# Kernel tuning notes

Hardware: AMD Instinct MI355X
Metric: run time of the kernel (lower is better)

Reference implementation:

```python
import jax, jax.numpy as jnp
import numpy as np
from jax import lax

IN_DIM = 128
B, H, W = 4, 64, 64


def setup_inputs() -> dict:
    key = jax.random.key(0)
    ks = jax.random.split(key, 11)
    C = IN_DIM
    c8 = C // 8
    s = lambda k, shape, scale: jax.random.normal(k, shape, dtype=jnp.float32) * scale
    return {
        "x": s(ks[0], (B, C, H, W), 1.0),
        "x_forward": s(ks[1], (B, C, H, W), 1.0),
        "x_backward": s(ks[2], (B, C, H, W), 1.0),
        # 1x1 conv weights stored as [out, in]
        "Wq": s(ks[3], (c8, C), C ** -0.5),
        "bq": jnp.zeros((c8,), jnp.float32),
        "Wk": s(ks[4], (c8, C), C ** -0.5),
        "bk": jnp.zeros((c8,), jnp.float32),
        "Wv": s(ks[5], (C, C), C ** -0.5),
        "bv": jnp.zeros((C,), jnp.float32),
        # 3x3 conv weight [out=C, in=2C, kh, kw]
        "Wf": s(ks[6], (C, 2 * C, 3, 3), (2 * C * 9) ** -0.5),
        "bf": jnp.zeros((C,), jnp.float32),
    }


def _conv1x1(x, w, b):
    # x: [B,C,H,W], w: [O,C] -> [B,O,H,W]
    return jnp.einsum("bchw,oc->bohw", x, w) + b[None, :, None, None]


def reference(x, x_forward, x_backward, Wq, bq, Wk, bk, Wv, bv, Wf, bf):
    Bb, C, Hh, Ww = x.shape
    HW = Hh * Ww
    query = _conv1x1(x_forward, Wq, bq).reshape(Bb, -1, HW)   # [B,c8,HW]
    key = _conv1x1(x, Wk, bk).reshape(Bb, -1, HW)             # [B,c8,HW]
    value = _conv1x1(x_backward, Wv, bv).reshape(Bb, C, HW)   # [B,C,HW]

    # att_score[b, k_pos, q_pos] = key[b,:,k_pos] . query[b,:,q_pos]
    att_score = jnp.einsum("bck,bcq->bkq", key, query)        # [B,HW,HW]
    max_value = jnp.max(att_score, axis=-1)                   # [B,HW]
    idx = jnp.argmax(att_score, axis=-1)                      # [B,HW] int

    selected_value = jnp.take_along_axis(value, idx[:, None, :], axis=2)
    selected_value = selected_value.reshape(Bb, C, Hh, Ww)
    max_value = max_value.reshape(Bb, 1, Hh, Ww)

    front_res = jnp.concatenate([x, selected_value], axis=1)  # [B,2C,H,W]
    front_res = lax.conv_general_dilated(
        front_res, Wf, window_strides=(1, 1), padding="SAME",
        dimension_numbers=("NCHW", "OIHW", "NCHW"),
    ) + bf[None, :, None, None]
    front_res = front_res * max_value
    return x + front_res
```

## Files before the change

### kernel.cpp

```cpp
#include <hip/hip_runtime.h>

#define HW 4096
#define CC 128
#define MARGIN 2e-3f

typedef unsigned short ushort_t;
typedef unsigned int uint_t;
typedef __attribute__((ext_vector_type(8))) short short8;
typedef __attribute__((ext_vector_type(4))) float f32x4;

__device__ __forceinline__ float dot4(float4 a, float4 b) {
    return (a.x*b.x + a.y*b.y) + (a.z*b.z + a.w*b.w);
}

__device__ __forceinline__ ushort_t f2bf(float f) {
    union { float f; uint_t u; } cv; cv.f = f;
    uint_t r = cv.u + 0x7fffu + ((cv.u >> 16) & 1u);
    return (ushort_t)(r >> 16);
}

__device__ __forceinline__ float bf2f(ushort_t h) {
    union { uint_t u; float f; } cv; cv.u = ((uint_t)h) << 16;
    return cv.f;
}

__device__ __forceinline__ void store16(ushort_t* dst, const ushort_t* s) {
    union { ushort_t s[8]; uint4 v; } a, b;
    #pragma unroll
    for (int j = 0; j < 8; j++) { a.s[j] = s[j]; b.s[j] = s[8+j]; }
    *(uint4*)dst = a.v;
    *(uint4*)(dst + 8) = b.v;
}

__device__ __forceinline__ void gl2lds16(const ushort_t* g, ushort_t* l) {
    __builtin_amdgcn_global_load_lds(
        (const __attribute__((address_space(1))) unsigned int*)g,
        (__attribute__((address_space(3))) unsigned int*)l, 16, 0, 0);
}

__global__ __launch_bounds__(256) void prep_kernel(
    const float* __restrict__ x, const float* __restrict__ xf,
    const float* __restrict__ Wq, const float* __restrict__ bq,
    const float* __restrict__ Wk, const float* __restrict__ bk,
    const float* __restrict__ Wf,
    float* __restrict__ Qt, float* __restrict__ Kt,
    ushort_t* __restrict__ Qs, ushort_t* __restrict__ KB,
    ushort_t* __restrict__ xsel, ushort_t* __restrict__ Wt)
{
    __shared__ __align__(16) unsigned char smem[16704];
    int bid = blockIdx.x;
    int tid = threadIdx.x;

    if (bid < 128) {
        bool isQ = bid < 64;
        const float* src  = isQ ? xf : x;
        const float* W    = isQ ? Wq : Wk;
        const float* bias = isQ ? bq : bk;

        int pg = (bid & 63) * 256 + tid;
        int b = pg >> 12, p = pg & 4095;
        const float* sp = src + ((size_t)b << 19) + p;

        float acc[16];
        #pragma unroll
        for (int o = 0; o < 16; o++) acc[o] = bias[o];

        for (int c4 = 0; c4 < 128; c4 += 4) {
            float x0 = sp[(size_t)(c4+0) << 12];
            float x1 = sp[(size_t)(c4+1) << 12];
            float x2 = sp[(size_t)(c4+2) << 12];
            float x3 = sp[(size_t)(c4+3) << 12];
            #pragma unroll
            for (int o = 0; o < 16; o++) {
                float4 w = *(const float4*)&W[o*128 + c4];
                acc[o] += w.x*x0 + w.y*x1 + w.z*x2 + w.w*x3;
            }
        }

        float* dstF = isQ ? Qt : Kt;
        float4* df = (float4*)(dstF + (size_t)pg * 16);
        df[0] = make_float4(acc[0],acc[1],acc[2],acc[3]);
        df[1] = make_float4(acc[4],acc[5],acc[6],acc[7]);
        df[2] = make_float4(acc[8],acc[9],acc[10],acc[11]);
        df[3] = make_float4(acc[12],acc[13],acc[14],acc[15]);

        ushort_t h[16], m[16], l[16];
        #pragma unroll
        for (int d = 0; d < 16; d++) {
            h[d] = f2bf(acc[d]);
            float r1 = acc[d] - bf2f(h[d]);
            m[d] = f2bf(r1);
            l[d] = f2bf(r1 - bf2f(m[d]));
        }
        if (isQ) {
            ushort_t* o_ = Qs + (size_t)pg*64;
            store16(o_,      h);
            store16(o_ + 16, m);
            store16(o_ + 32, h);
            store16(o_ + 48, l);
        } else {
            int u = b*256 + (p >> 4);
            int n = p & 15;
            ushort_t* o_ = KB + (size_t)u*1536 + n*32;
            store16(o_,        h); store16(o_ + 16,   h);
            store16(o_ + 512,  m); store16(o_ + 528,  m);
            store16(o_ + 1024, l); store16(o_ + 1040, h);
        }
    } else if (bid < 384) {
        ushort_t* sT = (ushort_t*)smem;
        int xbid = bid - 128;
        int b = xbid >> 6, y = xbid & 63;
        int cq = tid >> 6, xx = tid & 63;
        const float* src = x + ((size_t)b << 19) + (y << 6) + xx;
        #pragma unroll 4
        for (int k = 0; k < 32; k++) {
            int c = cq*32 + k;
            sT[xx*130 + c] = f2bf(src[(size_t)c << 12]);
        }
        __syncthreads();
        uint_t* dst = (uint_t*)(xsel + ((size_t)(b*4356 + (y+1)*66 + 1))*256);
        #pragma unroll
        for (int k = 0; k < 16; k++) {
            int idx = k*256 + tid;
            int s = idx >> 6, u = idx & 63;
            uint_t v = *(const uint_t*)&sT[s*130 + u*2];
            dst[s*128 + u] = v;
        }
    } else if (bid < 514) {
        int g = (bid - 384) * 256 + tid;
        if (g < 33280) {
            int b = g / 8320;
            int rem = g - b * 8320;
            int si = rem >> 5;
            int ch = rem & 31;
            int y, xx;
            if (si < 66)      { y = 0;  xx = si; }
            else if (si < 132){ y = 65; xx = si - 66; }
            else { int t = si - 132; y = 1 + (t >> 1); xx = (t & 1) ? 65 : 0; }
            int site = y * 66 + xx;
            uint4* dst = (uint4*)(xsel + ((size_t)(b*4356 + site))*256);
            dst[ch] = make_uint4(0,0,0,0);
        }
    } else {
        int t = (bid - 514) * 256 + tid;
        if (t < 36864) {
            int cg = t & 3;
            int o = (t >> 2) & 31;
            int tc = t >> 7;
            int tap = tc % 9;
            int rest = tc / 9;
            int cb = rest & 7, og = rest >> 3;
            union { ushort_t s[8]; uint4 v; } pk;
            #pragma unroll
            for (int j = 0; j < 8; j++) {
                int ci = cg*8 + j;
                pk.s[j] = f2bf(Wf[(size_t)(og*32 + o)*2304 + (cb*32 + ci)*9 + tap]);
            }
            *(uint4*)(Wt + (size_t)t*8) = pk.v;
        }
    }
}

__global__ __launch_bounds__(256) void v_kernel(
    const float* __restrict__ xb, const float* __restrict__ Wv,
    const float* __restrict__ bv, float* __restrict__ V)
{
    __shared__ __align__(16) float sW[32*128];
    int bid = blockIdx.x;
    int b = bid >> 6, og = (bid >> 4) & 3, pt = bid & 15;
    int tid = threadIdx.x;
    for (int e = tid; e < 4096; e += 256) sW[e] = Wv[og*4096 + e];
    __syncthreads();

    int oz = tid >> 7, pz = tid & 127;
    int p0 = pt*256 + pz, p1 = p0 + 128;
    const float* sp = xb + ((size_t)b << 19);

    float acc0[16], acc1[16];
    #pragma unroll
    for (int j = 0; j < 16; j++) { acc0[j] = 0.f; acc1[j] = 0.f; }

    for (int c4 = 0; c4 < 128; c4 += 4) {
        float a0 = sp[((size_t)(c4+0)<<12) + p0], a1 = sp[((size_t)(c4+1)<<12) + p0];
        float a2 = sp[((size_t)(c4+2)<<12) + p0], a3 = sp[((size_t)(c4+3)<<12) + p0];
        float b0 = sp[((size_t)(c4+0)<<12) + p1], b1 = sp[((size_t)(c4+1)<<12) + p1];
        float b2 = sp[((size_t)(c4+2)<<12) + p1], b3 = sp[((size_t)(c4+3)<<12) + p1];
        #pragma unroll
        for (int j = 0; j < 16; j++) {
            float4 w = *(const float4*)&sW[(oz*16 + j)*128 + c4];
            acc0[j] += w.x*a0 + w.y*a1 + w.z*a2 + w.w*a3;
            acc1[j] += w.x*b0 + w.y*b1 + w.z*b2 + w.w*b3;
        }
    }
    int obase = og*32 + oz*16;
    float* r0 = V + ((size_t)((b<<12) + p0))*128 + obase;
    float* r1 = V + ((size_t)((b<<12) + p1))*128 + obase;
    #pragma unroll
    for (int jq = 0; jq < 4; jq++) {
        float b0v = bv[obase + jq*4 + 0], b1v = bv[obase + jq*4 + 1];
        float b2v = bv[obase + jq*4 + 2], b3v = bv[obase + jq*4 + 3];
        *(float4*)(r0 + jq*4) = make_float4(acc0[jq*4]+b0v, acc0[jq*4+1]+b1v, acc0[jq*4+2]+b2v, acc0[jq*4+3]+b3v);
        *(float4*)(r1 + jq*4) = make_float4(acc1[jq*4]+b0v, acc1[jq*4+1]+b1v, acc1[jq*4+2]+b2v, acc1[jq*4+3]+b3v);
    }
}

__global__ __launch_bounds__(512, 2) void att_kernel(
    const ushort_t* __restrict__ Qs, const ushort_t* __restrict__ KB,
    float* __restrict__ maxv, int* __restrict__ idxv,
    int* __restrict__ gN, int* __restrict__ gList)
{
    __shared__ float sM1[64*33];
    __shared__ int   sI1[64*33];
    __shared__ float sM2[64*33];

    int bid = blockIdx.x;
    int kg = bid & 63, b = bid >> 6;
    int tid = threadIdx.x;
    int wave = tid >> 6, lane = tid & 63;
    int l15 = lane & 15, quad = lane >> 4;

    short8 Bf[4][3];
    const ushort_t* kb = KB + ((size_t)((b*256 + kg*4)*3))*512 + l15*32 + quad*8;
    #pragma unroll
    for (int t = 0; t < 4; t++)
        #pragma unroll
        for (int p = 0; p < 3; p++)
            Bf[t][p] = *(const short8*)(kb + (size_t)(t*3 + p)*512);

    const ushort_t* qbase = Qs + ((size_t)(b*4096 + wave*512 + l15))*64 + quad*8;

    float m1[4], m2[4]; int i1[4];
    #pragma unroll
    for (int t = 0; t < 4; t++) { m1[t] = -1e30f; m2[t] = -1e30f; i1[t] = 0; }

    for (int it = 0; it < 32; it++) {
        const ushort_t* aptr = qbase + it*1024;
        short8 A1 = *(const short8*)aptr;
        short8 A2 = *(const short8*)(aptr + 32);
        f32x4 acc[4];
        #pragma unroll
        for (int t = 0; t < 4; t++) {
            acc[t] = (f32x4)0.f;
            acc[t] = __builtin_amdgcn_mfma_f32_16x16x32_bf16(A1, Bf[t][0], acc[t], 0, 0, 0);
            acc[t] = __builtin_amdgcn_mfma_f32_16x16x32_bf16(A1, Bf[t][1], acc[t], 0, 0, 0);
            acc[t] = __builtin_amdgcn_mfma_f32_16x16x32_bf16(A2, Bf[t][2], acc[t], 0, 0, 0);
        }
        int q0 = wave*512 + it*16 + quad*4;
        #pragma unroll
        for (int r = 0; r < 4; r++) {
            int cand = q0 + r;
            #pragma unroll
            for (int t = 0; t < 4; t++) {
                float d = acc[t][r];
                float old1 = m1[t];
                bool gt = d > old1;
                m1[t] = gt ? d : old1;
                i1[t] = gt ? cand : i1[t];
                m2[t] = __builtin_amdgcn_fmed3f(d, old1, m2[t]);
            }
        }
    }

    #pragma unroll
    for (int t = 0; t < 4; t++) {
        int kl_ = t*16 + l15;
        int slot = wave*4 + quad;
        sM1[kl_*33 + slot] = m1[t];
        sI1[kl_*33 + slot] = i1[t];
        sM2[kl_*33 + slot] = m2[t];
    }
    __syncthreads();
    if (tid < 64) {
        float M1 = -1e30f; int I1 = 0x7fffffff;
        for (int s = 0; s < 32; s++) {
            float m = sM1[tid*33 + s]; int i = sI1[tid*33 + s];
            if (m > M1 || (m == M1 && i < I1)) { M1 = m; I1 = i; }
        }
        float M2 = -1e30f;
        for (int s = 0; s < 32; s++) {
            float m = sM1[tid*33 + s]; int i = sI1[tid*33 + s];
            float cnd = (i == I1) ? sM2[tid*33 + s] : m;
            M2 = fmaxf(M2, cnd);
        }
        int row = (b << 12) + kg*64 + tid;
        maxv[row] = M1; idxv[row] = I1;
        if (M1 - M2 < MARGIN) {
            int p = atomicAdd(gN, 1);
            gList[p] = row;
        }
    }
}

__global__ __launch_bounds__(256) void fixup2_kernel(
    const float* __restrict__ Qt, const float* __restrict__ Kt,
    const int* __restrict__ gN, const int* __restrict__ gList,
    float* __restrict__ maxv, int* __restrict__ idxv)
{
    __shared__ float sRm[256];
    __shared__ int   sRi[256];
    int n = *gN;
    int tid = threadIdx.x;
    for (int e = blockIdx.x; e < n; e += 64) {
        int r2 = gList[e];
        int b2 = r2 >> 12, k2 = r2 & 4095;
        const float4* Kp = (const float4*)(Kt + ((size_t)(b2*4096 + k2))*16);
        float4 ka = Kp[0], kbv = Kp[1], kc = Kp[2], kd = Kp[3];
        const float4* Qp = (const float4*)(Qt + ((size_t)b2*4096)*16);
        float m = -1e30f; int i = 0;
        #pragma unroll 4
        for (int j = 0; j < 16; j++) {
            int q = tid*16 + j;
            float4 qa = Qp[q*4+0], qb = Qp[q*4+1], qc = Qp[q*4+2], qd = Qp[q*4+3];
            float d = (dot4(ka,qa) + dot4(kbv,qb)) + (dot4(kc,qc) + dot4(kd,qd));
            if (d > m) { m = d; i = q; }
        }
        sRm[tid] = m; sRi[tid] = i;
        __syncthreads();
        #pragma unroll
        for (int s = 128; s > 0; s >>= 1) {
            if (tid < s) {
                float mo = sRm[tid+s]; int io = sRi[tid+s];
                if (mo > sRm[tid] || (mo == sRm[tid] && io < sRi[tid])) {
                    sRm[tid] = mo; sRi[tid] = io;
                }
            }
            __syncthreads();
        }
        if (tid == 0) { maxv[r2] = sRm[0]; idxv[r2] = sRi[0]; }
        __syncthreads();
    }
}

__global__ __launch_bounds__(256) void gather_kernel(
    const float* __restrict__ V, const int* __restrict__ idxv,
    ushort_t* __restrict__ xsel)
{
    int bid = blockIdx.x;
    int b = bid >> 6, pt = bid & 63;
    int tid = threadIdx.x;
    int pp = tid >> 2, cq = tid & 3;
    int p = pt*64 + pp;
    int ip = idxv[(b << 12) + p];
    const float* vrow = V + ((size_t)((b << 12) + ip))*128 + cq*32;
    int site = ((p >> 6) + 1)*66 + (p & 63) + 1;
    ushort_t* dst = xsel + ((size_t)(b*4356 + site))*256 + 128 + cq*32;
    #pragma unroll
    for (int k = 0; k < 4; k++) {
        float4 a = *(const float4*)(vrow + k*8);
        float4 c = *(const float4*)(vrow + k*8 + 4);
        union { ushort_t s[8]; uint4 v; } pk;
        pk.s[0] = f2bf(a.x); pk.s[1] = f2bf(a.y); pk.s[2] = f2bf(a.z); pk.s[3] = f2bf(a.w);
        pk.s[4] = f2bf(c.x); pk.s[5] = f2bf(c.y); pk.s[6] = f2bf(c.z); pk.s[7] = f2bf(c.w);
        *(uint4*)(dst + k*8) = pk.v;
    }
}

__global__ __launch_bounds__(256) void conv_kernel(
    const float* __restrict__ x, const ushort_t* __restrict__ xsel,
    const ushort_t* __restrict__ Wt, const float* __restrict__ bf,
    const float* __restrict__ maxv, float* __restrict__ out)
{
    __shared__ __align__(16) ushort_t sIn[336*32];
    __shared__ __align__(16) ushort_t sW[9*32*32];

    int bid = blockIdx.x;
    int og = bid & 3, tx = (bid >> 2) & 3, ty = (bid >> 4) & 3, b = bid >> 6;
    int tid = threadIdx.x;
    int wave = tid >> 6, lane = tid & 63;
    int l15 = lane & 15, quad = lane >> 4;

    const ushort_t* xsel_base = xsel + ((size_t)(b*4356 + (ty*16)*66 + tx*16))*256;
    const ushort_t* wt_base   = Wt + (size_t)og*8*9216;

    f32x4 acc[4][2];
    #pragma unroll
    for (int mi = 0; mi < 4; mi++)
        #pragma unroll
        for (int ni = 0; ni < 2; ni++) acc[mi][ni] = (f32x4)0.f;

    int l4q = lane >> 2, l4 = lane & 3;

    for (int cb = 0; cb < 8; cb++) {
        if (cb) __syncthreads();
        for (int r = wave; r < 21; r += 4) {
            int site = r*16 + l4q;
            int iy = site / 18, ix = site - iy*18;
            const ushort_t* g = xsel_base + (size_t)(iy*66 + ix)*256 + cb*32 + l4*8;
            gl2lds16(g, &sIn[r*512]);
        }
        for (int r = wave; r < 18; r += 4) {
            const ushort_t* g = wt_base + (size_t)cb*9216 + r*512 + lane*8;
            gl2lds16(g, &sW[r*512]);
        }
        __syncthreads();

        #pragma unroll
        for (int tap = 0; tap < 9; tap++) {
            const int dy = tap / 3, dx = tap % 3;
            short8 B0 = *(const short8*)&sW[(tap*32 +      l15)*32 + quad*8];
            short8 B1 = *(const short8*)&sW[(tap*32 + 16 + l15)*32 + quad*8];
            #pragma unroll
            for (int mi = 0; mi < 4; mi++) {
                int row = wave*4 + mi + dy;
                short8 A = *(const short8*)&sIn[(row*18 + l15 + dx)*32 + quad*8];
                acc[mi][0] = __builtin_amdgcn_mfma_f32_16x16x32_bf16(A, B0, acc[mi][0], 0, 0, 0);
                acc[mi][1] = __builtin_amdgcn_mfma_f32_16x16x32_bf16(A, B1, acc[mi][1], 0, 0, 0);
            }
        }
    }

    int y0 = ty*16, x0 = tx*16;
    const float* xb_ = x   + ((size_t)b << 19);
    float*       ob  = out + ((size_t)b << 19);
    const float* mxb = maxv + (b << 12);
    #pragma unroll
    for (int mi = 0; mi < 4; mi++) {
        int y = y0 + wave*4 + mi;
        int p = (y << 6) + x0 + quad*4;
        float4 mv = *(const float4*)&mxb[p];
        #pragma unroll
        for (int ni = 0; ni < 2; ni++) {
            int o = og*32 + ni*16 + l15;
            float bfo = bf[o];
            float4 xv = *(const float4*)&xb_[((size_t)o << 12) + p];
            float4 r;
            r.x = xv.x + mv.x * (acc[mi][ni][0] + bfo);
            r.y = xv.y + mv.y * (acc[mi][ni][1] + bfo);
            r.z = xv.z + mv.z * (acc[mi][ni][2] + bfo);
            r.w = xv.w + mv.w * (acc[mi][ni][3] + bfo);
            *(float4*)&ob[((size_t)o << 12) + p] = r;
        }
    }
}

extern "C" void kernel_launch(void* const* d_in, const int* in_sizes, int n_in,
                              void* d_out, int out_size, void* d_ws, size_t ws_size,
                              hipStream_t stream) {
    (void)in_sizes; (void)n_in; (void)out_size; (void)ws_size;
    const float* x  = (const float*)d_in[0];
    const float* xf = (const float*)d_in[1];
    const float* xb = (const float*)d_in[2];
    const float* Wq = (const float*)d_in[3];
    const float* bq = (const float*)d_in[4];
    const float* Wk = (const float*)d_in[5];
    const float* bk = (const float*)d_in[6];
    const float* Wv = (const float*)d_in[7];
    const float* bv = (const float*)d_in[8];
    const float* Wf = (const float*)d_in[9];
    const float* bf = (const float*)d_in[10];
    float* out = (float*)d_out;

    float* ws   = (float*)d_ws;
    float* Qt   = ws;
    float* Kt   = Qt + 262144;
    float* V    = Kt + 262144;
    float* mx   = V  + 2097152;
    int*   idxv = (int*)(mx + 16384);
    int*   gN   = (int*)(idxv + 16384);
    int*   gList= gN + 4;
    ushort_t* Qs   = (ushort_t*)(gList + 16384);
    ushort_t* KB   = Qs + 1048576;
    ushort_t* xsel = KB + 1572864;
    ushort_t* Wt   = xsel + 4460544;

    hipMemsetAsync(gN, 0, sizeof(int), stream);
    hipLaunchKernelGGL(prep_kernel,   dim3(658), dim3(256), 0, stream,
                       x, xf, Wq, bq, Wk, bk, Wf, Qt, Kt, Qs, KB, xsel, Wt);
    hipLaunchKernelGGL(v_kernel,      dim3(256), dim3(256), 0, stream, xb, Wv, bv, V);
    hipLaunchKernelGGL(att_kernel,    dim3(256), dim3(512), 0, stream, Qs, KB, mx, idxv, gN, gList);
    hipLaunchKernelGGL(fixup2_kernel, dim3(64),  dim3(256), 0, stream, Qt, Kt, gN, gList, mx, idxv);
    hipLaunchKernelGGL(gather_kernel, dim3(256), dim3(256), 0, stream, V, idxv, xsel);
    hipLaunchKernelGGL(conv_kernel,   dim3(256), dim3(256), 0, stream, x, xsel, Wt, bf, mx, out);
}
```

Baseline: 204.7 us.

## Fold V projection into prep kernel and split Q/K channel reduction across threads

Merges the separate value-projection kernel into the prep kernel as extra blocks, so one launch covers Q/K, V, padding, transpose and weight repacking. The Q/K projection now uses twice as many blocks, with each half-block reducing half the channels and combining partial sums through shared memory. V blocks are re-tiled to 8 outputs per thread over 1024 blocks. The aim is to remove a launch and its serialization and to raise parallelism in the small projection stages. In exchange it adds a block-level sync, reloads x_backward once per output group, and leaves half the Q/K threads idle during the epilogue.

```diff
diff --git a/kernel.cpp b/kernel.cpp
--- a/kernel.cpp
+++ b/kernel.cpp
@@ -39,11 +39,12 @@
 }
 
 __global__ __launch_bounds__(256) void prep_kernel(
-    const float* __restrict__ x, const float* __restrict__ xf,
+    const float* __restrict__ x, const float* __restrict__ xf, const float* __restrict__ xb,
     const float* __restrict__ Wq, const float* __restrict__ bq,
     const float* __restrict__ Wk, const float* __restrict__ bk,
+    const float* __restrict__ Wv, const float* __restrict__ bv,
     const float* __restrict__ Wf,
-    float* __restrict__ Qt, float* __restrict__ Kt,
+    float* __restrict__ Qt, float* __restrict__ Kt, float* __restrict__ V,
     ushort_t* __restrict__ Qs, ushort_t* __restrict__ KB,
     ushort_t* __restrict__ xsel, ushort_t* __restrict__ Wt)
 {
@@ -51,19 +52,87 @@
     int bid = blockIdx.x;
     int tid = threadIdx.x;
 
-    if (bid < 128) {
-        bool isQ = bid < 64;
+    if (bid < 256) {
+        bool isQ = bid < 128;
+        int sub = bid & 127;
+        int b = sub >> 5, pt = sub & 31;
         const float* src  = isQ ? xf : x;
         const float* W    = isQ ? Wq : Wk;
         const float* bias = isQ ? bq : bk;
-
-        int pg = (bid & 63) * 256 + tid;
-        int b = pg >> 12, p = pg & 4095;
-        const float* sp = src + ((size_t)b << 19) + p;
+        int ph = tid >> 7, pl = tid & 127;
+        int p = pt*128 + pl;
+        int pg = (b << 12) + p;
+        const float* sp = src + ((size_t)b << 19) + p + ((size_t)(ph*64) << 12);
 
         float acc[16];
         #pragma unroll
-        for (int o = 0; o < 16; o++) acc[o] = bias[o];
+        for (int o = 0; o < 16; o++) acc[o] = ph ? 0.f : bias[o];
+
+        for (int cc = 0; cc < 64; cc += 4) {
+            float x0 = sp[(size_t)(cc+0) << 12];
+            float x1 = sp[(size_t)(cc+1) << 12];
+            float x2 = sp[(size_t)(cc+2) << 12];
+            float x3 = sp[(size_t)(cc+3) << 12];
+            #pragma unroll
+            for (int o = 0; o < 16; o++) {
+                float4 w = *(const float4*)&W[o*128 + ph*64 + cc];
+                acc[o] += w.x*x0 + w.y*x1 + w.z*x2 + w.w*x3;
+            }
+        }
+
+        float* sAcc = (float*)smem;
+        if (ph) {
+            #pragma unroll
+            for (int o = 0; o < 16; o++) sAcc[pl*17 + o] = acc[o];
+        }
+        __syncthreads();
+        if (!ph) {
+            #pragma unroll
+            for (int o = 0; o < 16; o++) acc[o] += sAcc[pl*17 + o];
+
+            float* dstF = isQ ? Qt : Kt;
+            float4* df = (float4*)(dstF + (size_t)pg * 16);
+            df[0] = make_float4(acc[0],acc[1],acc[2],acc[3]);
+            df[1] = make_float4(acc[4],acc[5],acc[6],acc[7]);
+            df[2] = make_float4(acc[8],acc[9],acc[10],acc[11]);
+            df[3] = make_float4(acc[12],acc[13],acc[14],acc[15]);
+
+            ushort_t h[16], m[16], l[16];
+            #pragma unroll
+            for (int d = 0; d < 16; d++) {
+                h[d] = f2bf(acc[d]);
+                float r1 = acc[d] - bf2f(h[d]);
+                m[d] = f2bf(r1);
+                l[d] = f2bf(r1 - bf2f(m[d]));
+            }
+            if (isQ) {
+                ushort_t* o_ = Qs + (size_t)pg*64;
+                store16(o_,      h);
+                store16(o_ + 16, m);
+                store16(o_ + 32, h);
+                store16(o_ + 48, l);
+            } else {
+                int u = b*256 + (p >> 4);
+                int n = p & 15;
+                ushort_t* o_ = KB + (size_t)u*1536 + n*32;
+                store16(o_,        h); store16(o_ + 16,   h);
+                store16(o_ + 512,  m); store16(o_ + 528,  m);
+                store16(o_ + 1024, l); store16(o_ + 1040, h);
+            }
+        }
+    } else if (bid < 1280) {
+        int vbid = bid - 256;
+        int b = vbid >> 8, og = (vbid >> 4) & 15, pt = vbid & 15;
+        float* sW = (float*)smem;
+        for (int e = tid; e < 1024; e += 256) sW[e] = Wv[og*1024 + e];
+        __syncthreads();
+
+        int p = pt*256 + tid;
+        const float* sp = xb + ((size_t)b << 19) + p;
+
+        float acc[8];
+        #pragma unroll
+        for (int j = 0; j < 8; j++) acc[j] = 0.f;
 
         for (int c4 = 0; c4 < 128; c4 += 4) {
             float x0 = sp[(size_t)(c4+0) << 12];
@@ -71,44 +140,21 @@
             float x2 = sp[(size_t)(c4+2) << 12];
             float x3 = sp[(size_t)(c4+3) << 12];
             #pragma unroll
-            for (int o = 0; o < 16; o++) {
-                float4 w = *(const float4*)&W[o*128 + c4];
-                acc[o] += w.x*x0 + w.y*x1 + w.z*x2 + w.w*x3;
-            }
-        }
-
-        float* dstF = isQ ? Qt : Kt;
-        float4* df = (float4*)(dstF + (size_t)pg * 16);
-        df[0] = make_float4(acc[0],acc[1],acc[2],acc[3]);
-        df[1] = make_float4(acc[4],acc[5],acc[6],acc[7]);
-        df[2] = make_float4(acc[8],acc[9],acc[10],acc[11]);
-        df[3] = make_float4(acc[12],acc[13],acc[14],acc[15]);
-
-        ushort_t h[16], m[16], l[16];
-        #pragma unroll
-        for (int d = 0; d < 16; d++) {
-            h[d] = f2bf(acc[d]);
-            float r1 = acc[d] - bf2f(h[d]);
-            m[d] = f2bf(r1);
-            l[d] = f2bf(r1 - bf2f(m[d]));
-        }
-        if (isQ) {
-            ushort_t* o_ = Qs + (size_t)pg*64;
-            store16(o_,      h);
-            store16(o_ + 16, m);
-            store16(o_ + 32, h);
-            store16(o_ + 48, l);
-        } else {
-            int u = b*256 + (p >> 4);
-            int n = p & 15;
-            ushort_t* o_ = KB + (size_t)u*1536 + n*32;
-            store16(o_,        h); store16(o_ + 16,   h);
-            store16(o_ + 512,  m); store16(o_ + 528,  m);
-            store16(o_ + 1024, l); store16(o_ + 1040, h);
-        }
-    } else if (bid < 384) {
+            for (int j = 0; j < 8; j++) {
+                float4 w = *(const float4*)&sW[j*128 + c4];
+                acc[j] += w.x*x0 + w.y*x1 + w.z*x2 + w.w*x3;
+            }
+        }
+        float* vr = V + ((size_t)((b << 12) + p))*128 + og*8;
+        float4 r0 = make_float4(acc[0]+bv[og*8+0], acc[1]+bv[og*8+1],
+                                acc[2]+bv[og*8+2], acc[3]+bv[og*8+3]);
+        float4 r1 = make_float4(acc[4]+bv[og*8+4], acc[5]+bv[og*8+5],
+                                acc[6]+bv[og*8+6], acc[7]+bv[og*8+7]);
+        *(float4*)vr = r0;
+        *(float4*)(vr + 4) = r1;
+    } else if (bid < 1536) {
         ushort_t* sT = (ushort_t*)smem;
-        int xbid = bid - 128;
+        int xbid = bid - 1280;
         int b = xbid >> 6, y = xbid & 63;
         int cq = tid >> 6, xx = tid & 63;
         const float* src = x + ((size_t)b << 19) + (y << 6) + xx;
@@ -126,8 +172,8 @@
             uint_t v = *(const uint_t*)&sT[s*130 + u*2];
             dst[s*128 + u] = v;
         }
-    } else if (bid < 514) {
-        int g = (bid - 384) * 256 + tid;
+    } else if (bid < 1666) {
+        int g = (bid - 1536) * 256 + tid;
         if (g < 33280) {
             int b = g / 8320;
             int rem = g - b * 8320;
@@ -142,7 +188,7 @@
             dst[ch] = make_uint4(0,0,0,0);
         }
     } else {
-        int t = (bid - 514) * 256 + tid;
+        int t = (bid - 1666) * 256 + tid;
         if (t < 36864) {
             int cg = t & 3;
             int o = (t >> 2) & 31;
@@ -158,49 +204,6 @@
             }
             *(uint4*)(Wt + (size_t)t*8) = pk.v;
         }
-    }
-}
-
-__global__ __launch_bounds__(256) void v_kernel(
-    const float* __restrict__ xb, const float* __restrict__ Wv,
-    const float* __restrict__ bv, float* __restrict__ V)
-{
-    __shared__ __align__(16) float sW[32*128];
-    int bid = blockIdx.x;
-    int b = bid >> 6, og = (bid >> 4) & 3, pt = bid & 15;
-    int tid = threadIdx.x;
-    for (int e = tid; e < 4096; e += 256) sW[e] = Wv[og*4096 + e];
-    __syncthreads();
-
-    int oz = tid >> 7, pz = tid & 127;
-    int p0 = pt*256 + pz, p1 = p0 + 128;
-    const float* sp = xb + ((size_t)b << 19);
-
-    float acc0[16], acc1[16];
-    #pragma unroll
-    for (int j = 0; j < 16; j++) { acc0[j] = 0.f; acc1[j] = 0.f; }
-
-    for (int c4 = 0; c4 < 128; c4 += 4) {
-        float a0 = sp[((size_t)(c4+0)<<12) + p0], a1 = sp[((size_t)(c4+1)<<12) + p0];
-        float a2 = sp[((size_t)(c4+2)<<12) + p0], a3 = sp[((size_t)(c4+3)<<12) + p0];
-        float b0 = sp[((size_t)(c4+0)<<12) + p1], b1 = sp[((size_t)(c4+1)<<12) + p1];
-        float b2 = sp[((size_t)(c4+2)<<12) + p1], b3 = sp[((size_t)(c4+3)<<12) + p1];
-        #pragma unroll
-        for (int j = 0; j < 16; j++) {
-            float4 w = *(const float4*)&sW[(oz*16 + j)*128 + c4];
-            acc0[j] += w.x*a0 + w.y*a1 + w.z*a2 + w.w*a3;
-            acc1[j] += w.x*b0 + w.y*b1 + w.z*b2 + w.w*b3;
-        }
-    }
-    int obase = og*32 + oz*16;
-    float* r0 = V + ((size_t)((b<<12) + p0))*128 + obase;
-    float* r1 = V + ((size_t)((b<<12) + p1))*128 + obase;
-    #pragma unroll
-    for (int jq = 0; jq < 4; jq++) {
-        float b0v = bv[obase + jq*4 + 0], b1v = bv[obase + jq*4 + 1];
-        float b2v = bv[obase + jq*4 + 2], b3v = bv[obase + jq*4 + 3];
-        *(float4*)(r0 + jq*4) = make_float4(acc0[jq*4]+b0v, acc0[jq*4+1]+b1v, acc0[jq*4+2]+b2v, acc0[jq*4+3]+b3v);
-        *(float4*)(r1 + jq*4) = make_float4(acc1[jq*4]+b0v, acc1[jq*4+1]+b1v, acc1[jq*4+2]+b2v, acc1[jq*4+3]+b3v);
     }
 }
 
@@ -464,9 +467,9 @@
     ushort_t* Wt   = xsel + 4460544;
 
     hipMemsetAsync(gN, 0, sizeof(int), stream);
-    hipLaunchKernelGGL(prep_kernel,   dim3(658), dim3(256), 0, stream,
-                       x, xf, Wq, bq, Wk, bk, Wf, Qt, Kt, Qs, KB, xsel, Wt);
-    hipLaunchKernelGGL(v_kernel,      dim3(256), dim3(256), 0, stream, xb, Wv, bv, V);
+    hipLaunchKernelGGL(prep_kernel,   dim3(1810), dim3(256), 0, stream,
+                       x, xf, xb, Wq, bq, Wk, bk, Wv, bv, Wf,
+                       Qt, Kt, V, Qs, KB, xsel, Wt);
     hipLaunchKernelGGL(att_kernel,    dim3(256), dim3(512), 0, stream, Qs, KB, mx, idxv, gN, gList);
     hipLaunchKernelGGL(fixup2_kernel, dim3(64),  dim3(256), 0, stream, Qt, Kt, gN, gList, mx, idxv);
     hipLaunchKernelGGL(gather_kernel, dim3(256), dim3(256), 0, stream, V, idxv, xsel);
```

Result: faster. 173.6 us (-15.2%).
